# Kernel tuning notes

Hardware: AMD Instinct MI355X
Metric: run time of the kernel (lower is better)

The kernel has to match this reference:

```python
import jax, jax.numpy as jnp
import numpy as np

N, E, B = 10000, 160000, 64
H, M, NE = 64, 64, 10
NIN = NE + 1
L = 16  # (max_ell+1)^2 spherical-harmonic components, max_ell=3
NUM_LAYERS = 2
AVG_NEIGH = 16.0
NORM = 4.0  # normalization_factor
EPS = 1e-9

silu = jax.nn.silu


def sph_harm(u):
    # component-normalized real spherical harmonics l=0..3 of unit vectors u [E,3]
    x, y, z = u[..., 0], u[..., 1], u[..., 2]
    xx, yy, zz = x * x, y * y, z * z
    return jnp.stack([
        jnp.ones_like(x),
        1.7320508 * x, 1.7320508 * y, 1.7320508 * z,
        3.8729833 * x * y, 3.8729833 * y * z, 1.1180340 * (3.0 * zz - 1.0),
        3.8729833 * x * z, 1.9364917 * (xx - yy),
        2.0916500 * y * (3.0 * xx - yy), 10.2469508 * x * y * z,
        1.6201852 * y * (5.0 * zz - 1.0), 1.3228757 * z * (5.0 * zz - 3.0),
        1.6201852 * x * (5.0 * zz - 1.0), 5.1234754 * (xx - yy) * z,
        2.0916500 * x * (xx - 3.0 * yy),
    ], axis=-1)


def setup_inputs() -> dict:
    key = jax.random.key(0)
    ks = jax.random.split(key, 24)
    inp = {}
    inp["positions"] = jax.random.normal(ks[0], (N, 3), jnp.float32) * 3.0
    inp["node_attrs"] = jax.random.uniform(ks[1], (N, NE), jnp.float32)
    inp["t"] = jax.random.uniform(ks[2], (B, 1), jnp.float32)
    inp["shifts"] = jnp.zeros((E, 3), jnp.float32)
    inp["batch"] = jnp.sort(jax.random.randint(ks[3], (N,), 0, B))
    inp["edge_index"] = jax.random.randint(ks[4], (2, E), 0, N)

    def w(k, shape, fan_in):
        return (jax.random.normal(k, shape, jnp.float32) / np.float32(np.sqrt(fan_in)))

    inp["W_emb"] = w(ks[5], (NIN, H), NIN)
    inp["b_emb"] = jnp.zeros((H,), jnp.float32)
    inp["W_out"] = w(ks[6], (H, NIN), H)
    inp["b_out"] = jnp.zeros((NIN,), jnp.float32)
    inp["Wr1"] = w(ks[7], (NUM_LAYERS, 1, H), 1)
    inp["br1"] = jnp.zeros((NUM_LAYERS, H), jnp.float32)
    inp["Wr2"] = w(ks[8], (NUM_LAYERS, H, H), H)
    inp["W_up"] = w(ks[9], (NUM_LAYERS, H, H), H)
    inp["W_mix"] = w(ks[10], (NUM_LAYERS, H, H), H)
    inp["W_prod"] = w(ks[11], (NUM_LAYERS, H, H), H)
    inp["Wro1"] = w(ks[12], (NUM_LAYERS, H, M), H)
    inp["bro1"] = jnp.zeros((NUM_LAYERS, M), jnp.float32)
    inp["Wro2"] = w(ks[13], (NUM_LAYERS, M, H), M)
    inp["Wg"] = w(ks[14], (NUM_LAYERS, H, H), H)
    inp["wv"] = w(ks[15], (NUM_LAYERS, H), H)
    inp["Wmlp1"] = w(ks[16], (NUM_LAYERS, 2 * H, H), 2 * H)
    inp["bmlp1"] = jnp.zeros((NUM_LAYERS, H), jnp.float32)
    inp["Wmlp2"] = w(ks[17], (NUM_LAYERS, H, H), H)
    inp["bmlp2"] = jnp.zeros((NUM_LAYERS, H), jnp.float32)
    return inp


def reference(positions, node_attrs, t, shifts, batch, edge_index,
              W_emb, b_emb, W_out, b_out,
              Wr1, br1, Wr2, W_up, W_mix, W_prod,
              Wro1, bro1, Wro2, Wg, wv,
              Wmlp1, bmlp1, Wmlp2, bmlp2):
    snd, rcv = edge_index[0], edge_index[1]

    def edges(p):
        v = p[rcv] - p[snd] + shifts          # [E,3]
        return v, jnp.linalg.norm(v, axis=-1, keepdims=True)

    na = node_attrs / NORM
    h = jnp.concatenate([na, t[batch]], axis=-1) @ W_emb + b_emb   # [N,H]
    nf = jnp.zeros((N, H, L), h.dtype).at[:, :, 0].set(h)          # scalars -> l=0 slot
    pos0 = positions
    pos = positions
    vec, lengths = edges(pos)

    for i in range(NUM_LAYERS):
        u = vec / (jnp.linalg.norm(vec, axis=-1, keepdims=True) + EPS)
        Y = sph_harm(u)                                            # [E,L]
        # radial MLP on edge lengths -> per-edge channel weights
        r = silu(lengths @ Wr1[i] + br1[i]) @ Wr2[i]               # [E,H]
        nf_up = jnp.einsum('nhl,hk->nkl', nf, W_up[i])             # channel mix (equivariant)
        # depthwise tensor product: (radial * sender scalar) x Y, then scatter-sum
        msg = (r * nf_up[snd, :, 0])[:, :, None] * Y[:, None, :]   # [E,H,L]
        agg = jax.ops.segment_sum(msg, rcv, num_segments=N) / AVG_NEIGH
        a = jnp.einsum('nhl,hk->nkl', agg, W_mix[i])
        # symmetric contraction (correlation=3): equivariant scalar-gated polynomial
        s = a[:, :, 0:1]
        nf = jnp.einsum('nhl,hk->nkl', a * (1.0 + s + s * s), W_prod[i])
        # nonlinear readout: scalar MLP + gated vector head
        sc = nf[:, :, 0]                                           # [N,H]
        v3 = nf[:, :, 1:4]                                         # [N,H,3]
        scalars = silu(sc @ Wro1[i] + bro1[i]) @ Wro2[i]           # [N,H]
        gate = silu(sc @ Wg[i])                                    # [N,H]
        vout = jnp.einsum('nhc,h->nc', v3 * gate[:, :, None], wv[i])  # [N,3]
        pos = pos + vout
        h = h + silu(jnp.concatenate([h, scalars], axis=-1) @ Wmlp1[i] + bmlp1[i]) @ Wmlp2[i] + bmlp2[i]
        vec, lengths = edges(pos)

    pred = h @ W_out + b_out                                       # [N,NIN]
    counts = jax.ops.segment_sum(jnp.ones((N, 1), pos.dtype), batch, num_segments=B)
    means = jax.ops.segment_sum(pos, batch, num_segments=B) / jnp.maximum(counts, 1.0)
    pred_pos = (pos - means[batch]) - pos0                         # remove_mean - positions_0
    return pred[:, :-1], pred_pos
```

## Files before the change

kernel.cpp:

```cpp
#include <hip/hip_runtime.h>

#define NN 10000
#define NEDGE 160000
#define NBATCH 64

static constexpr size_t OFF_POS   = 0;
static constexpr size_t OFF_H     = 30016;
static constexpr size_t OFF_NF0   = OFF_H   + 640000;
static constexpr size_t OFF_NUP   = OFF_NF0 + 640000;
static constexpr size_t OFF_V3    = OFF_NUP + 640000;
static constexpr size_t OFF_Q1    = OFF_V3  + 1920000;
static constexpr size_t OFF_AGG   = OFF_Q1  + 640000;
static constexpr size_t OFF_WW    = OFF_AGG + 2560000;
static constexpr size_t OFF_WY    = OFF_WW  + 10240000;
static constexpr size_t OFF_ESLOT = OFF_WY  + 640000;
static constexpr size_t OFF_CSR   = OFF_ESLOT + 160000;
static constexpr size_t OFF_CNT   = OFF_CSR + 10016;
static constexpr size_t OFF_CUR   = OFF_CNT + 10016;
static constexpr size_t OFF_BACC  = OFF_CUR + 10016;
static constexpr size_t WS_END    = OFF_BACC + 256;

__device__ __forceinline__ float silu_f(float x) {
  return x / (1.0f + __expf(-x));
}

__global__ __launch_bounds__(256) void k_embed_count_up(
    const float* __restrict__ pos_in, const float* __restrict__ na,
    const float* __restrict__ t, const int* __restrict__ batch,
    const float* __restrict__ Wemb, const float* __restrict__ bemb,
    const float* __restrict__ Wup0,
    float* __restrict__ h, float* __restrict__ nf0, float* __restrict__ pos_cur,
    float* __restrict__ nfup0,
    const int* __restrict__ ei, int* __restrict__ counts) {
  if (blockIdx.x >= 2500) {
    int e = (blockIdx.x - 2500) * 256 + threadIdx.x;
    atomicAdd(&counts[ei[NEDGE + e]], 1);
    return;
  }
  __shared__ float sx[4][64];
  int tid = blockIdx.x * 256 + threadIdx.x;
  int n = tid >> 6, k = tid & 63;
  int w = threadIdx.x >> 6;
  float acc = bemb[k];
  const float* arow = na + n * 10;
#pragma unroll
  for (int j = 0; j < 10; ++j)
    acc = fmaf(arow[j] * 0.25f, Wemb[j * 64 + k], acc);
  acc = fmaf(t[batch[n]], Wemb[10 * 64 + k], acc);
  h[tid] = acc;
  nf0[tid] = acc;
  if (k < 3) pos_cur[n * 3 + k] = pos_in[n * 3 + k];
  sx[w][k] = acc;
  __syncthreads();
  float up = 0.f;
  for (int hh = 0; hh < 64; ++hh)
    up = fmaf(sx[w][hh], Wup0[hh * 64 + k], up);
  nfup0[tid] = up;
}

__global__ __launch_bounds__(1024) void k_scan(const int* __restrict__ counts,
                                               int* __restrict__ offs) {
  __shared__ int part[1024];
  int tid = threadIdx.x;
  int base = tid * 10;
  int local[10];
  int s = 0;
#pragma unroll
  for (int j = 0; j < 10; ++j) {
    int idx = base + j;
    int v = (idx < NN) ? counts[idx] : 0;
    local[j] = s;
    s += v;
  }
  part[tid] = s;
  __syncthreads();
  for (int d = 1; d < 1024; d <<= 1) {
    int v = (tid >= d) ? part[tid - d] : 0;
    __syncthreads();
    part[tid] += v;
    __syncthreads();
  }
  int excl = (tid == 0) ? 0 : part[tid - 1];
#pragma unroll
  for (int j = 0; j < 10; ++j) {
    int idx = base + j;
    if (idx < NN) offs[idx] = excl + local[j];
  }
  if (tid == 1023) offs[NN] = excl + s;
}

__global__ __launch_bounds__(256) void k_scatter(
    const int* __restrict__ ei, const int* __restrict__ offs,
    int* __restrict__ cursor, int* __restrict__ eslot) {
  int e = blockIdx.x * 256 + threadIdx.x;
  int r = ei[NEDGE + e];
  int slot = atomicAdd(&cursor[r], 1);
  eslot[e] = offs[r] + slot;
}

__global__ __launch_bounds__(256) void k_edge(
    const int* __restrict__ ei, const float* __restrict__ shifts,
    const float* __restrict__ pos, const float* __restrict__ nfup0,
    const float* __restrict__ Wr1, const float* __restrict__ br1,
    const float* __restrict__ Wr2, const int* __restrict__ eslot,
    float* __restrict__ w_s, float4* __restrict__ y_s) {
  int e = blockIdx.x * 256 + threadIdx.x;
  int s = ei[e], r = ei[NEDGE + e];
  float vx = pos[r * 3 + 0] - pos[s * 3 + 0] + shifts[e * 3 + 0];
  float vy = pos[r * 3 + 1] - pos[s * 3 + 1] + shifts[e * 3 + 1];
  float vz = pos[r * 3 + 2] - pos[s * 3 + 2] + shifts[e * 3 + 2];
  float len = sqrtf(vx * vx + vy * vy + vz * vz);
  float inv = 1.0f / (len + 1e-9f);
  int slot = eslot[e];
  const float c1 = 1.7320508f * 0.0625f;
  y_s[slot] = make_float4(0.0625f, c1 * vx * inv, c1 * vy * inv, c1 * vz * inv);

  const float4* W2q = (const float4*)Wr2;
  float4 acc[16];
#pragma unroll
  for (int j = 0; j < 16; ++j) acc[j] = make_float4(0.f, 0.f, 0.f, 0.f);
  for (int hh = 0; hh < 64; ++hh) {
    float x = fmaf(len, Wr1[hh], br1[hh]);
    float sl = silu_f(x);
#pragma unroll
    for (int j = 0; j < 16; ++j) {
      float4 wq = W2q[hh * 16 + j];
      acc[j].x = fmaf(sl, wq.x, acc[j].x);
      acc[j].y = fmaf(sl, wq.y, acc[j].y);
      acc[j].z = fmaf(sl, wq.z, acc[j].z);
      acc[j].w = fmaf(sl, wq.w, acc[j].w);
    }
  }
  const float4* nrow = (const float4*)(nfup0 + (size_t)s * 64);
  float4* wrow = (float4*)(w_s + (size_t)slot * 64);
#pragma unroll
  for (int j = 0; j < 16; ++j) {
    float4 nv = nrow[j];
    float4 o;
    o.x = acc[j].x * nv.x; o.y = acc[j].y * nv.y;
    o.z = acc[j].z * nv.z; o.w = acc[j].w * nv.w;
    wrow[j] = o;
  }
}

__global__ __launch_bounds__(256) void k_gather(
    const int* __restrict__ offs, const float* __restrict__ w_s,
    const float4* __restrict__ y_s, float4* __restrict__ agg) {
  int gtid = blockIdx.x * 256 + threadIdx.x;
  int n = gtid >> 6;
  int lane = threadIdx.x & 63;
  int beg = offs[n], end = offs[n + 1];
  float a0 = 0.f, a1 = 0.f, a2 = 0.f, a3 = 0.f;
  for (int j = beg; j < end; ++j) {
    float w = w_s[(size_t)j * 64 + lane];
    float4 y = y_s[j];
    a0 = fmaf(w, y.x, a0);
    a1 = fmaf(w, y.y, a1);
    a2 = fmaf(w, y.z, a2);
    a3 = fmaf(w, y.w, a3);
  }
  agg[(size_t)n * 64 + lane] = make_float4(a0, a1, a2, a3);
}

__global__ __launch_bounds__(512) void k_mix_prod(
    const float4* __restrict__ agg, const float* __restrict__ Wmix,
    const float* __restrict__ Wprod, float* __restrict__ nf0,
    float* __restrict__ v3, const float* __restrict__ Wup_next,
    float* __restrict__ nfup0) {
  __shared__ float sMix[4096];
  __shared__ float sProd[4096];
  __shared__ float sUp[4096];
  __shared__ float4 xb[8][64];
  for (int i = threadIdx.x; i < 4096; i += 512) { sMix[i] = Wmix[i]; sProd[i] = Wprod[i]; }
  if (Wup_next)
    for (int i = threadIdx.x; i < 4096; i += 512) sUp[i] = Wup_next[i];
  int w = threadIdx.x >> 6, lane = threadIdx.x & 63;
  __syncthreads();
  for (int it = 0; it < 5; ++it) {
    int n = it * 2000 + blockIdx.x * 8 + w;
    xb[w][lane] = agg[(size_t)n * 64 + lane];
    __syncthreads();
    float4 a = make_float4(0.f, 0.f, 0.f, 0.f);
    for (int hh = 0; hh < 64; ++hh) {
      float4 x = xb[w][hh];
      float m = sMix[hh * 64 + lane];
      a.x = fmaf(x.x, m, a.x); a.y = fmaf(x.y, m, a.y);
      a.z = fmaf(x.z, m, a.z); a.w = fmaf(x.w, m, a.w);
    }
    float sv = a.x;
    float f = 1.0f + sv + sv * sv;
    a.x *= f; a.y *= f; a.z *= f; a.w *= f;
    __syncthreads();
    xb[w][lane] = a;
    __syncthreads();
    float4 nf = make_float4(0.f, 0.f, 0.f, 0.f);
    for (int hh = 0; hh < 64; ++hh) {
      float4 x = xb[w][hh];
      float m = sProd[hh * 64 + lane];
      nf.x = fmaf(x.x, m, nf.x); nf.y = fmaf(x.y, m, nf.y);
      nf.z = fmaf(x.z, m, nf.z); nf.w = fmaf(x.w, m, nf.w);
    }
    nf0[(size_t)n * 64 + lane] = nf.x;
    v3[(size_t)n * 192 + lane * 3 + 0] = nf.y;
    v3[(size_t)n * 192 + lane * 3 + 1] = nf.z;
    v3[(size_t)n * 192 + lane * 3 + 2] = nf.w;
    if (Wup_next) {
      __syncthreads();
      xb[w][lane].x = nf.x;
      __syncthreads();
      float up = 0.f;
      for (int hh = 0; hh < 64; ++hh)
        up = fmaf(xb[w][hh].x, sUp[hh * 64 + lane], up);
      nfup0[(size_t)n * 64 + lane] = up;
    }
    __syncthreads();
  }
}

__global__ __launch_bounds__(512) void k_readout_mlp(
    const float* __restrict__ nf0, const float* __restrict__ v3,
    const float* __restrict__ Wro1, const float* __restrict__ bro1,
    const float* __restrict__ Wg, const float* __restrict__ wvv,
    const float* __restrict__ Wro2,
    const float* __restrict__ Wmlp1, const float* __restrict__ bmlp1,
    const float* __restrict__ Wmlp2, const float* __restrict__ bmlp2,
    float* __restrict__ pos, float* __restrict__ h) {
  __shared__ float sR[4096];
  __shared__ float sG[4096];
  __shared__ float sRo2[4096];
  __shared__ float sM1[8192];
  __shared__ float sM2[4096];
  __shared__ float sx[8][64], sq[8][64], ssc[8][64], sh[8][64], su[8][64];
  __shared__ float swv[64];
  for (int i = threadIdx.x; i < 4096; i += 512) {
    sR[i] = Wro1[i]; sG[i] = Wg[i]; sRo2[i] = Wro2[i]; sM2[i] = Wmlp2[i];
  }
  for (int i = threadIdx.x; i < 8192; i += 512) sM1[i] = Wmlp1[i];
  if (threadIdx.x < 64) swv[threadIdx.x] = wvv[threadIdx.x];
  int w = threadIdx.x >> 6, lane = threadIdx.x & 63;
  __syncthreads();
  for (int it = 0; it < 5; ++it) {
    int n = it * 2000 + blockIdx.x * 8 + w;
    sx[w][lane] = nf0[(size_t)n * 64 + lane];
    sh[w][lane] = h[(size_t)n * 64 + lane];
    __syncthreads();
    float q = bro1[lane];
    float g = 0.f;
    for (int hh = 0; hh < 64; ++hh) {
      float x = sx[w][hh];
      q = fmaf(x, sR[hh * 64 + lane], q);
      g = fmaf(x, sG[hh * 64 + lane], g);
    }
    q = silu_f(q);
    g = silu_f(g);
    float gw = g * swv[lane];
    float p0 = v3[(size_t)n * 192 + lane * 3 + 0] * gw;
    float p1 = v3[(size_t)n * 192 + lane * 3 + 1] * gw;
    float p2 = v3[(size_t)n * 192 + lane * 3 + 2] * gw;
#pragma unroll
    for (int m = 32; m > 0; m >>= 1) {
      p0 += __shfl_xor(p0, m);
      p1 += __shfl_xor(p1, m);
      p2 += __shfl_xor(p2, m);
    }
    if (lane == 0) {
      pos[n * 3 + 0] += p0;
      pos[n * 3 + 1] += p1;
      pos[n * 3 + 2] += p2;
    }
    sq[w][lane] = q;
    __syncthreads();
    float sc = 0.f;
    for (int m = 0; m < 64; ++m) sc = fmaf(sq[w][m], sRo2[m * 64 + lane], sc);
    ssc[w][lane] = sc;
    __syncthreads();
    float u = bmlp1[lane];
    for (int j = 0; j < 64; ++j) u = fmaf(sh[w][j], sM1[j * 64 + lane], u);
    for (int j = 0; j < 64; ++j) u = fmaf(ssc[w][j], sM1[(64 + j) * 64 + lane], u);
    u = silu_f(u);
    su[w][lane] = u;
    __syncthreads();
    float ho = sh[w][lane] + bmlp2[lane];
    for (int m = 0; m < 64; ++m) ho = fmaf(su[w][m], sM2[m * 64 + lane], ho);
    h[(size_t)n * 64 + lane] = ho;
    __syncthreads();
  }
}

__global__ __launch_bounds__(256) void k_pred(
    const float* __restrict__ h, const float* __restrict__ Wout,
    const float* __restrict__ bout, float* __restrict__ out) {
  __shared__ float sW[704];
  for (int i = threadIdx.x; i < 704; i += 256) sW[i] = Wout[i];
  __syncthreads();
  int n = blockIdx.x * 256 + threadIdx.x;
  if (n >= NN) return;
  float acc[10];
#pragma unroll
  for (int j = 0; j < 10; ++j) acc[j] = bout[j];
  const float* row = h + (size_t)n * 64;
  for (int hh = 0; hh < 64; ++hh) {
    float hv = row[hh];
#pragma unroll
    for (int j = 0; j < 10; ++j) acc[j] = fmaf(hv, sW[hh * 11 + j], acc[j]);
  }
  float* orow = out + (size_t)n * 10;
#pragma unroll
  for (int j = 0; j < 10; ++j) orow[j] = acc[j];
}

__global__ __launch_bounds__(256) void k_batch(
    const int* __restrict__ batch, const float* __restrict__ pos,
    float* __restrict__ bacc) {
  int n = blockIdx.x * 256 + threadIdx.x;
  int lane = threadIdx.x & 63;
  bool valid = n < NN;
  int b = valid ? batch[n] : -1;
  float p0 = valid ? pos[n * 3 + 0] : 0.f;
  float p1 = valid ? pos[n * 3 + 1] : 0.f;
  float p2 = valid ? pos[n * 3 + 2] : 0.f;
  float c  = valid ? 1.f : 0.f;
#pragma unroll
  for (int d = 1; d < 64; d <<= 1) {
    float q0 = __shfl_down(p0, d);
    float q1 = __shfl_down(p1, d);
    float q2 = __shfl_down(p2, d);
    float qc = __shfl_down(c, d);
    int bd   = __shfl_down(b, d);
    if (lane + d < 64 && bd == b) { p0 += q0; p1 += q1; p2 += q2; c += qc; }
  }
  int bprev = __shfl_up(b, 1);
  bool head = valid && (lane == 0 || bprev != b);
  if (head) {
    atomicAdd(&bacc[b * 4 + 0], p0);
    atomicAdd(&bacc[b * 4 + 1], p1);
    atomicAdd(&bacc[b * 4 + 2], p2);
    atomicAdd(&bacc[b * 4 + 3], c);
  }
}

__global__ __launch_bounds__(256) void k_predpos(
    const int* __restrict__ batch, const float* __restrict__ pos,
    const float* __restrict__ pos0, const float* __restrict__ bacc,
    float* __restrict__ out) {
  int n = blockIdx.x * 256 + threadIdx.x;
  if (n >= NN) return;
  int b = batch[n];
  float cnt = fmaxf(bacc[b * 4 + 3], 1.0f);
#pragma unroll
  for (int c = 0; c < 3; ++c)
    out[NN * 10 + n * 3 + c] = pos[n * 3 + c] - bacc[b * 4 + c] / cnt - pos0[n * 3 + c];
}

extern "C" void kernel_launch(void* const* d_in, const int* in_sizes, int n_in,
                              void* d_out, int out_size, void* d_ws, size_t ws_size,
                              hipStream_t stream) {
  const float* positions = (const float*)d_in[0];
  const float* node_attrs = (const float*)d_in[1];
  const float* t_in = (const float*)d_in[2];
  const float* shifts = (const float*)d_in[3];
  const int* batch = (const int*)d_in[4];
  const int* edge_index = (const int*)d_in[5];
  const float* W_emb = (const float*)d_in[6];
  const float* b_emb = (const float*)d_in[7];
  const float* W_out = (const float*)d_in[8];
  const float* b_out = (const float*)d_in[9];
  const float* Wr1 = (const float*)d_in[10];
  const float* br1 = (const float*)d_in[11];
  const float* Wr2 = (const float*)d_in[12];
  const float* W_up = (const float*)d_in[13];
  const float* W_mix = (const float*)d_in[14];
  const float* W_prod = (const float*)d_in[15];
  const float* Wro1 = (const float*)d_in[16];
  const float* bro1 = (const float*)d_in[17];
  const float* Wro2 = (const float*)d_in[18];
  const float* Wg = (const float*)d_in[19];
  const float* wv = (const float*)d_in[20];
  const float* Wmlp1 = (const float*)d_in[21];
  const float* bmlp1 = (const float*)d_in[22];
  const float* Wmlp2 = (const float*)d_in[23];
  const float* bmlp2 = (const float*)d_in[24];

  float* ws = (float*)d_ws;
  float* pos_cur = ws + OFF_POS;
  float* hbuf    = ws + OFF_H;
  float* nf0     = ws + OFF_NF0;
  float* nfup0   = ws + OFF_NUP;
  float* v3      = ws + OFF_V3;
  float4* agg    = (float4*)(ws + OFF_AGG);
  float* w_s     = ws + OFF_WW;
  float4* y_s    = (float4*)(ws + OFF_WY);
  int* eslot     = (int*)(ws + OFF_ESLOT);
  int* csroff    = (int*)(ws + OFF_CSR);
  int* counts    = (int*)(ws + OFF_CNT);
  int* cursor    = (int*)(ws + OFF_CUR);
  float* bacc    = ws + OFF_BACC;

  hipMemsetAsync(counts, 0, (WS_END - OFF_CNT) * sizeof(float), stream);

  k_embed_count_up<<<3125, 256, 0, stream>>>(positions, node_attrs, t_in, batch,
                                             W_emb, b_emb, W_up,
                                             hbuf, nf0, pos_cur, nfup0,
                                             edge_index, counts);
  k_scan<<<1, 1024, 0, stream>>>(counts, csroff);
  k_scatter<<<625, 256, 0, stream>>>(edge_index, csroff, cursor, eslot);

  for (int i = 0; i < 2; ++i) {
    k_edge<<<625, 256, 0, stream>>>(edge_index, shifts, pos_cur, nfup0,
                                    Wr1 + i * 64, br1 + i * 64, Wr2 + i * 4096,
                                    eslot, w_s, y_s);
    k_gather<<<2500, 256, 0, stream>>>(csroff, w_s, y_s, agg);
    k_mix_prod<<<250, 512, 0, stream>>>(agg, W_mix + i * 4096, W_prod + i * 4096,
                                        nf0, v3,
                                        (i == 0) ? (W_up + 4096) : nullptr, nfup0);
    k_readout_mlp<<<250, 512, 0, stream>>>(nf0, v3, Wro1 + i * 4096, bro1 + i * 64,
                                           Wg + i * 4096, wv + i * 64,
                                           Wro2 + i * 4096,
                                           Wmlp1 + i * 8192, bmlp1 + i * 64,
                                           Wmlp2 + i * 4096, bmlp2 + i * 64,
                                           pos_cur, hbuf);
  }

  k_pred<<<40, 256, 0, stream>>>(hbuf, W_out, b_out, (float*)d_out);
  k_batch<<<40, 256, 0, stream>>>(batch, pos_cur, bacc);
  k_predpos<<<40, 256, 0, stream>>>(batch, pos_cur, positions, bacc, (float*)d_out);
}
```

Before: 400.7 us.

## Register-tile radial MLP in k_edge over 4 edges with LDS-staged weights

The edge kernel now stages the radial-MLP weights (Wr2, Wr1, br1) in shared memory. Each thread handles 4 edges and half of the 64 output channels, so every loaded weight float4 is reused across 4 edges. The grid is halved to cover 512 edges per block. Silu evaluations are duplicated across the two halves, and fewer blocks (313) may reduce occupancy and latency hiding on a 256-CU device.

```diff
diff --git a/kernel.cpp b/kernel.cpp
--- a/kernel.cpp
+++ b/kernel.cpp
@@ -104,42 +104,79 @@
     const float* __restrict__ Wr1, const float* __restrict__ br1,
     const float* __restrict__ Wr2, const int* __restrict__ eslot,
     float* __restrict__ w_s, float4* __restrict__ y_s) {
-  int e = blockIdx.x * 256 + threadIdx.x;
-  int s = ei[e], r = ei[NEDGE + e];
-  float vx = pos[r * 3 + 0] - pos[s * 3 + 0] + shifts[e * 3 + 0];
-  float vy = pos[r * 3 + 1] - pos[s * 3 + 1] + shifts[e * 3 + 1];
-  float vz = pos[r * 3 + 2] - pos[s * 3 + 2] + shifts[e * 3 + 2];
-  float len = sqrtf(vx * vx + vy * vy + vz * vz);
-  float inv = 1.0f / (len + 1e-9f);
-  int slot = eslot[e];
-  const float c1 = 1.7320508f * 0.0625f;
-  y_s[slot] = make_float4(0.0625f, c1 * vx * inv, c1 * vy * inv, c1 * vz * inv);
-
-  const float4* W2q = (const float4*)Wr2;
-  float4 acc[16];
-#pragma unroll
-  for (int j = 0; j < 16; ++j) acc[j] = make_float4(0.f, 0.f, 0.f, 0.f);
+  __shared__ float4 sW[1024];
+  __shared__ float sW1[64];
+  __shared__ float sB1[64];
+  {
+    const float4* W4 = (const float4*)Wr2;
+    for (int i = threadIdx.x; i < 1024; i += 256) sW[i] = W4[i];
+    if (threadIdx.x < 64) { sW1[threadIdx.x] = Wr1[threadIdx.x]; sB1[threadIdx.x] = br1[threadIdx.x]; }
+  }
+  __syncthreads();
+  int half = threadIdx.x >> 7;
+  int sub  = threadIdx.x & 127;
+  int ebase = blockIdx.x * 512 + sub * 4;
+
+  float len[4]; int slot[4]; int snd[4]; bool v[4];
+#pragma unroll
+  for (int q = 0; q < 4; ++q) {
+    int e = ebase + q;
+    v[q] = e < NEDGE;
+    int ec = v[q] ? e : 0;
+    int s = ei[ec], r = ei[NEDGE + ec];
+    snd[q] = s;
+    float vx = pos[r * 3 + 0] - pos[s * 3 + 0] + shifts[ec * 3 + 0];
+    float vy = pos[r * 3 + 1] - pos[s * 3 + 1] + shifts[ec * 3 + 1];
+    float vz = pos[r * 3 + 2] - pos[s * 3 + 2] + shifts[ec * 3 + 2];
+    float l = sqrtf(vx * vx + vy * vy + vz * vz);
+    len[q] = l;
+    slot[q] = eslot[ec];
+    if (half == 0 && v[q]) {
+      float inv = 1.0f / (l + 1e-9f);
+      const float c1 = 1.7320508f * 0.0625f;
+      y_s[slot[q]] = make_float4(0.0625f, c1 * vx * inv, c1 * vy * inv, c1 * vz * inv);
+    }
+  }
+
+  float4 acc[4][8];
+#pragma unroll
+  for (int q = 0; q < 4; ++q)
+#pragma unroll
+    for (int j = 0; j < 8; ++j) acc[q][j] = make_float4(0.f, 0.f, 0.f, 0.f);
+
+  const float4* sWh = sW + half * 8;
   for (int hh = 0; hh < 64; ++hh) {
-    float x = fmaf(len, Wr1[hh], br1[hh]);
-    float sl = silu_f(x);
-#pragma unroll
-    for (int j = 0; j < 16; ++j) {
-      float4 wq = W2q[hh * 16 + j];
-      acc[j].x = fmaf(sl, wq.x, acc[j].x);
-      acc[j].y = fmaf(sl, wq.y, acc[j].y);
-      acc[j].z = fmaf(sl, wq.z, acc[j].z);
-      acc[j].w = fmaf(sl, wq.w, acc[j].w);
-    }
-  }
-  const float4* nrow = (const float4*)(nfup0 + (size_t)s * 64);
-  float4* wrow = (float4*)(w_s + (size_t)slot * 64);
-#pragma unroll
-  for (int j = 0; j < 16; ++j) {
-    float4 nv = nrow[j];
-    float4 o;
-    o.x = acc[j].x * nv.x; o.y = acc[j].y * nv.y;
-    o.z = acc[j].z * nv.z; o.w = acc[j].w * nv.w;
-    wrow[j] = o;
+    float w1 = sW1[hh], b1 = sB1[hh];
+    float sl[4];
+#pragma unroll
+    for (int q = 0; q < 4; ++q)
+      sl[q] = silu_f(fmaf(len[q], w1, b1));
+#pragma unroll
+    for (int j = 0; j < 8; ++j) {
+      float4 wq = sWh[hh * 16 + j];
+#pragma unroll
+      for (int q = 0; q < 4; ++q) {
+        acc[q][j].x = fmaf(sl[q], wq.x, acc[q][j].x);
+        acc[q][j].y = fmaf(sl[q], wq.y, acc[q][j].y);
+        acc[q][j].z = fmaf(sl[q], wq.z, acc[q][j].z);
+        acc[q][j].w = fmaf(sl[q], wq.w, acc[q][j].w);
+      }
+    }
+  }
+
+#pragma unroll
+  for (int q = 0; q < 4; ++q) {
+    if (!v[q]) continue;
+    const float4* nrow = (const float4*)(nfup0 + (size_t)snd[q] * 64) + half * 8;
+    float4* wrow = (float4*)(w_s + (size_t)slot[q] * 64) + half * 8;
+#pragma unroll
+    for (int j = 0; j < 8; ++j) {
+      float4 nv = nrow[j];
+      float4 o;
+      o.x = acc[q][j].x * nv.x; o.y = acc[q][j].y * nv.y;
+      o.z = acc[q][j].z * nv.z; o.w = acc[q][j].w * nv.w;
+      wrow[j] = o;
+    }
   }
 }
 
@@ -406,7 +443,7 @@
   k_scatter<<<625, 256, 0, stream>>>(edge_index, csroff, cursor, eslot);
 
   for (int i = 0; i < 2; ++i) {
-    k_edge<<<625, 256, 0, stream>>>(edge_index, shifts, pos_cur, nfup0,
+    k_edge<<<313, 256, 0, stream>>>(edge_index, shifts, pos_cur, nfup0,
                                     Wr1 + i * 64, br1 + i * 64, Wr2 + i * 4096,
                                     eslot, w_s, y_s);
     k_gather<<<2500, 256, 0, stream>>>(csroff, w_s, y_s, agg);
```

Result: slower. 419.7 us (+4.7%).
